# Optimization experiments

Hardware: AMD Instinct MI355X
Metric: run time of the kernel (lower is better)

Reference implementation:

```python
import jax, jax.numpy as jnp
import numpy as np

DIM = 64
N_ENTITY = 1000000
N_RELATION = 32
L = 2
B = 4096
K = 64


def setup_inputs() -> dict:
    key = jax.random.key(0)
    ks = jax.random.split(key, 24)
    s = 0.05
    d = DIM
    inp = {
        "items": jax.random.randint(ks[0], (B,), 0, N_ENTITY),
        "heads": jax.random.randint(ks[1], (L, B, K), 0, N_ENTITY),
        "relations": jax.random.randint(ks[2], (L, B, K), 0, N_RELATION),
        "tails": jax.random.randint(ks[3], (L, B, K), 0, N_ENTITY),
        # learned parameters
        "embedding": jax.random.normal(ks[4], (N_ENTITY, d), jnp.float32) * s,
        "transformer": jax.random.normal(ks[5], (N_RELATION, d), jnp.float32) * s,
        "attn_w": jax.random.normal(ks[6], (1, 3 * d), jnp.float32) * s,
        "attn_b": jax.random.normal(ks[7], (1,), jnp.float32) * s,
        "W_ih": jax.random.normal(ks[8], (d, d), jnp.float32) * s,
        "W_hh": jax.random.normal(ks[9], (d, d), jnp.float32) * s,
        "b_ih": jax.random.normal(ks[10], (d,), jnp.float32) * s,
        "b_hh": jax.random.normal(ks[11], (d,), jnp.float32) * s,
        "l1_w": jax.random.normal(ks[12], (d, 2 * d), jnp.float32) * s,
        "l1_b": jax.random.normal(ks[13], (d,), jnp.float32) * s,
        "l2_w": jax.random.normal(ks[14], (d, d), jnp.float32) * s,
        "l2_b": jax.random.normal(ks[15], (d,), jnp.float32) * s,
        "l3_w": jax.random.normal(ks[16], (d, d), jnp.float32) * s,
        "l3_b": jax.random.normal(ks[17], (d,), jnp.float32) * s,
        "lin_w": jax.random.normal(ks[18], (1, 2 * d), jnp.float32) * s,
        "lin_b": jax.random.normal(ks[19], (1,), jnp.float32) * s,
    }
    return inp


def _ncfg_forward(embedding, transformer, attn_w, attn_b, W_ih, W_hh, b_ih, b_hh,
                  l1_w, l1_b, l2_w, l2_b, l3_w, l3_b, lin_w, lin_b,
                  items, heads, relations, tails):
    o_sum = jnp.zeros((B, DIM), embedding.dtype)
    for l in range(L):
        h = embedding[heads[l]]          # [B, K, d]
        r = transformer[relations[l]]    # [B, K, d]
        tl = embedding[tails[l]]         # [B, K, d]
        hRt = jnp.concatenate([h, r, tl], axis=-1)                  # [B, K, 3d]
        pi = jax.nn.sigmoid(hRt @ attn_w.T + attn_b)                # [B, K, 1]
        pi = jax.nn.softmax(pi, axis=1)                             # softmax over neighbors
        # 2-step tanh RNN over seq (head, tail), h0 = 0
        h1 = jnp.tanh(h @ W_ih.T + b_ih + b_hh)                     # [B, K, d]
        h2 = jnp.tanh(tl @ W_ih.T + b_ih + h1 @ W_hh.T + b_hh)      # [B, K, d]
        o_sum = o_sum + (pi * h2).sum(axis=1)                       # [B, d]
    user_emb = o_sum
    item_emb = embedding[items]                                     # [B, d]
    # NCF head (dropout in eval mode = identity)
    ui = jnp.concatenate([user_emb, item_emb], axis=-1)             # [B, 2d]
    y = jax.nn.relu(ui @ l1_w.T + l1_b)
    y = jax.nn.relu(y @ l2_w.T + l2_b)
    y1 = jax.nn.sigmoid(y @ l3_w.T + l3_b)
    y2 = user_emb * item_emb
    out = jax.nn.sigmoid(jnp.concatenate([y1, y2], axis=-1) @ lin_w.T + lin_b)
    return out[:, 0]  # squeeze -> [B]


def reference(items, heads, relations, tails, embedding, transformer, attn_w, attn_b,
              W_ih, W_hh, b_ih, b_hh, l1_w, l1_b, l2_w, l2_b, l3_w, l3_b, lin_w, lin_b):
    return _ncfg_forward(embedding, transformer, attn_w, attn_b, W_ih, W_hh, b_ih, b_hh,
                         l1_w, l1_b, l2_w, l2_b, l3_w, l3_b, lin_w, lin_b,
                         items, heads, relations, tails)
```

## Files before the change

kernel.cpp:

```cpp
#include <hip/hip_runtime.h>
#include <hip/hip_bf16.h>
#include <cstdint>
#include <cstddef>

#define B_SZ 4096

typedef __attribute__((ext_vector_type(4))) float f32x4;
typedef __attribute__((ext_vector_type(8))) short sv8;
typedef __attribute__((ext_vector_type(8))) __bf16 bfv8;

__device__ __align__(16) short g_wf[2][8][64][8];
__device__ float g_bsum[64];
__device__ float g_reldot[32];

static __device__ __forceinline__ short f2bf(float x) {
  union { float f; unsigned u; } v; v.f = x;
  unsigned r = v.u + 0x7fffu + ((v.u >> 16) & 1u);
  return (short)(r >> 16);
}
static __device__ __forceinline__ short f2bfc(float x) {
  return (short)__builtin_bit_cast(unsigned short, __float2bfloat16(x));
}

static __device__ __forceinline__ f32x4 MFMA(sv8 a, sv8 b, f32x4 c) {
  return __builtin_amdgcn_mfma_f32_16x16x32_bf16(
      __builtin_bit_cast(bfv8, a), __builtin_bit_cast(bfv8, b), c, 0, 0, 0);
}

static __device__ __forceinline__ float fast_sigmoid(float x) {
  return __builtin_amdgcn_rcpf(1.f + __expf(-x));
}
static __device__ __forceinline__ float fast_tanh(float x) {
  const float e = __expf(2.f * x);
  return 1.f - 2.f * __builtin_amdgcn_rcpf(e + 1.f);
}
static __device__ __forceinline__ float dot4(f32x4 a, f32x4 b) {
  return a.x * b.x + a.y * b.y + a.z * b.z + a.w * b.w;
}
static __device__ __forceinline__ sv8 pack8(f32x4 a, f32x4 b) {
  sv8 f;
  f[0] = f2bfc(a.x); f[1] = f2bfc(a.y); f[2] = f2bfc(a.z); f[3] = f2bfc(a.w);
  f[4] = f2bfc(b.x); f[5] = f2bfc(b.y); f[6] = f2bfc(b.z); f[7] = f2bfc(b.w);
  return f;
}

__global__ __launch_bounds__(256) void ncfg_prep(
    const float* __restrict__ W_ih, const float* __restrict__ W_hh,
    const float* __restrict__ b_ih, const float* __restrict__ b_hh,
    const float* __restrict__ trf, const float* __restrict__ attn_w) {
  const int t = threadIdx.x;
  for (int q = t; q < 1024; q += 256) {
    const int m = q >> 9, f = (q >> 6) & 7, ln = q & 63;
    const int nt = f >> 1, kh = f & 1, fr = ln & 15, fg = ln >> 4;
    const float* W = m ? W_hh : W_ih;
    const float* src = W + (nt * 16 + fr) * 64 + kh * 32 + fg * 8;
    short* dst = &g_wf[m][f][ln][0];
    #pragma unroll
    for (int j = 0; j < 8; ++j) dst[j] = f2bf(src[j]);
  }
  if (t < 64) g_bsum[t] = b_ih[t] + b_hh[t];
  if (t < 32) {
    float s = 0.f;
    #pragma unroll 8
    for (int c = 0; c < 64; ++c) s += trf[t * 64 + c] * attn_w[64 + c];
    g_reldot[t] = s;
  }
}

__global__ __launch_bounds__(256, 6) void ncfg_neigh(
    const int* __restrict__ heads, const int* __restrict__ rels,
    const int* __restrict__ tails, const float* __restrict__ emb,
    const float* __restrict__ attn_w, const float* __restrict__ attn_b,
    float* __restrict__ opart) {
  const int t = threadIdx.x;
  const int lane = t & 63;
  const int w = t >> 6;
  const int fr = lane & 15;
  const int fg = lane >> 4;
  const int c0 = fg * 8;

  __shared__ __align__(16) short wlds[2][8][64][8];
  __shared__ __align__(16) float awlds[192];
  __shared__ float rlds[32];
  __shared__ __align__(16) short h1s[4][16 * 72];

  const size_t ibase = (size_t)blockIdx.x * 64;

  const int hi = heads[ibase + (w << 4) + fr];
  const int ti = tails[ibase + (w << 4) + fr];
  const int ri = rels[ibase + (w << 4) + fr];

  {
    const f32x4* s1 = (const f32x4*)&g_wf[0][0][0][0];
    f32x4* d1 = (f32x4*)&wlds[0][0][0][0];
    #pragma unroll
    for (int i = 0; i < 4; ++i) d1[t + i * 256] = s1[t + i * 256];
    if (t < 48) ((f32x4*)awlds)[t] = ((const f32x4*)attn_w)[t];
    if (t < 8) ((f32x4*)rlds)[t] = ((const f32x4*)g_reldot)[t];
  }

  float bsum[4];
  #pragma unroll
  for (int nt = 0; nt < 4; ++nt) bsum[nt] = g_bsum[nt * 16 + fr];
  const float ab0 = attn_b[0];

  const float* hr = emb + (size_t)hi * 64;
  const float* tr = emb + (size_t)ti * 64;
  const f32x4 h0 = *(const f32x4*)(hr + c0);
  const f32x4 h1 = *(const f32x4*)(hr + c0 + 4);
  const f32x4 h2 = *(const f32x4*)(hr + 32 + c0);
  const f32x4 h3 = *(const f32x4*)(hr + 32 + c0 + 4);
  const f32x4 t0 = *(const f32x4*)(tr + c0);
  const f32x4 t1 = *(const f32x4*)(tr + c0 + 4);
  const f32x4 t2 = *(const f32x4*)(tr + 32 + c0);
  const f32x4 t3 = *(const f32x4*)(tr + 32 + c0 + 4);

  __syncthreads();

  float ap = dot4(h0, *(const f32x4*)&awlds[c0]) +
             dot4(h1, *(const f32x4*)&awlds[c0 + 4]) +
             dot4(h2, *(const f32x4*)&awlds[32 + c0]) +
             dot4(h3, *(const f32x4*)&awlds[32 + c0 + 4]) +
             dot4(t0, *(const f32x4*)&awlds[128 + c0]) +
             dot4(t1, *(const f32x4*)&awlds[128 + c0 + 4]) +
             dot4(t2, *(const f32x4*)&awlds[160 + c0]) +
             dot4(t3, *(const f32x4*)&awlds[160 + c0 + 4]);
  ap += __shfl_xor(ap, 16);
  ap += __shfl_xor(ap, 32);

  const float e_own = __expf(fast_sigmoid(ap + rlds[ri] + ab0));
  float se = e_own;
  se += __shfl_xor(se, 1);
  se += __shfl_xor(se, 2);
  se += __shfl_xor(se, 4);
  se += __shfl_xor(se, 8);

  const sv8 ha0 = pack8(h0, h1), ha1 = pack8(h2, h3);
  const sv8 ta0 = pack8(t0, t1), ta1 = pack8(t2, t3);

  const f32x4 zz = {0.f, 0.f, 0.f, 0.f};

  f32x4 acc[4] = {zz, zz, zz, zz};
  #pragma unroll
  for (int nt = 0; nt < 4; ++nt)
    acc[nt] = MFMA(ha0, *(const sv8*)&wlds[0][nt * 2][lane][0], acc[nt]);
  #pragma unroll
  for (int nt = 0; nt < 4; ++nt)
    acc[nt] = MFMA(ha1, *(const sv8*)&wlds[0][nt * 2 + 1][lane][0], acc[nt]);
  #pragma unroll
  for (int nt = 0; nt < 4; ++nt)
    #pragma unroll
    for (int r = 0; r < 4; ++r)
      h1s[w][((fg << 2) + r) * 72 + nt * 16 + fr] =
          f2bfc(fast_tanh(acc[nt][r] + bsum[nt]));

  f32x4 ev;
  #pragma unroll
  for (int r = 0; r < 4; ++r) ev[r] = __shfl(e_own, (fg << 2) + r);

  f32x4 acc2[4] = {zz, zz, zz, zz};
  #pragma unroll
  for (int nt = 0; nt < 4; ++nt)
    acc2[nt] = MFMA(ta0, *(const sv8*)&wlds[0][nt * 2][lane][0], acc2[nt]);
  #pragma unroll
  for (int nt = 0; nt < 4; ++nt)
    acc2[nt] = MFMA(ta1, *(const sv8*)&wlds[0][nt * 2 + 1][lane][0], acc2[nt]);
  const sv8 a1 = *(const sv8*)&h1s[w][fr * 72 + c0];
  const sv8 a2 = *(const sv8*)&h1s[w][fr * 72 + 32 + c0];
  #pragma unroll
  for (int nt = 0; nt < 4; ++nt)
    acc2[nt] = MFMA(a1, *(const sv8*)&wlds[1][nt * 2][lane][0], acc2[nt]);
  #pragma unroll
  for (int nt = 0; nt < 4; ++nt)
    acc2[nt] = MFMA(a2, *(const sv8*)&wlds[1][nt * 2 + 1][lane][0], acc2[nt]);

  float* owp = (float*)&h1s[w][0];
  #pragma unroll
  for (int nt = 0; nt < 4; ++nt) {
    float s = ev.x * fast_tanh(acc2[nt][0] + bsum[nt]) +
              ev.y * fast_tanh(acc2[nt][1] + bsum[nt]) +
              ev.z * fast_tanh(acc2[nt][2] + bsum[nt]) +
              ev.w * fast_tanh(acc2[nt][3] + bsum[nt]);
    s += __shfl_xor(s, 16);
    s += __shfl_xor(s, 32);
    if (fg == 0) owp[nt * 16 + fr] = s;
  }
  if (lane == 0) owp[64] = se;

  __syncthreads();

  if (w == 0) {
    float o = 0.f, st = 0.f;
    #pragma unroll
    for (int q = 0; q < 4; ++q) {
      const float* p = (const float*)&h1s[q][0];
      o += p[lane];
      st += p[64];
    }
    opart[ibase + lane] = o * __builtin_amdgcn_rcpf(st);
  }
}

__global__ __launch_bounds__(256) void ncfg_head(
    const float* __restrict__ opart, const float* __restrict__ emb,
    const int* __restrict__ items, const float* __restrict__ l1_w,
    const float* __restrict__ l1_b, const float* __restrict__ l2_w,
    const float* __restrict__ l2_b, const float* __restrict__ l3_w,
    const float* __restrict__ l3_b, const float* __restrict__ lin_w,
    const float* __restrict__ lin_b, float* __restrict__ out) {
  const int wv = threadIdx.x >> 6;
  const int i = threadIdx.x & 63;
  const int b = blockIdx.x * 4 + wv;

  __shared__ float ui[4][128];
  __shared__ float yy[4][64];

  const float ue = opart[(size_t)b * 64 + i] +
                   opart[((size_t)B_SZ + b) * 64 + i];
  const float ie = emb[(size_t)items[b] * 64 + i];
  ui[wv][i] = ue;
  ui[wv][64 + i] = ie;
  __syncthreads();

  float acc = l1_b[i];
  {
    const float* wr = l1_w + i * 128;
    #pragma unroll
    for (int j = 0; j < 128; j += 4) {
      const f32x4 wvv = *(const f32x4*)(wr + j);
      const f32x4 uv = *(const f32x4*)&ui[wv][j];
      acc += wvv.x * uv.x + wvv.y * uv.y + wvv.z * uv.z + wvv.w * uv.w;
    }
  }
  float y = fmaxf(acc, 0.f);
  yy[wv][i] = y;
  __syncthreads();

  acc = l2_b[i];
  {
    const float* wr = l2_w + i * 64;
    #pragma unroll
    for (int j = 0; j < 64; j += 4) {
      const f32x4 wvv = *(const f32x4*)(wr + j);
      const f32x4 uv = *(const f32x4*)&yy[wv][j];
      acc += wvv.x * uv.x + wvv.y * uv.y + wvv.z * uv.z + wvv.w * uv.w;
    }
  }
  y = fmaxf(acc, 0.f);
  __syncthreads();
  yy[wv][i] = y;
  __syncthreads();

  acc = l3_b[i];
  {
    const float* wr = l3_w + i * 64;
    #pragma unroll
    for (int j = 0; j < 64; j += 4) {
      const f32x4 wvv = *(const f32x4*)(wr + j);
      const f32x4 uv = *(const f32x4*)&yy[wv][j];
      acc += wvv.x * uv.x + wvv.y * uv.y + wvv.z * uv.z + wvv.w * uv.w;
    }
  }
  const float y1 = fast_sigmoid(acc);
  const float y2 = ue * ie;

  float part = y1 * lin_w[i] + y2 * lin_w[64 + i];
  #pragma unroll
  for (int m = 1; m < 64; m <<= 1) part += __shfl_xor(part, m);
  if (i == 0) out[b] = fast_sigmoid(part + lin_b[0]);
}

extern "C" void kernel_launch(void* const* d_in, const int* in_sizes, int n_in,
                              void* d_out, int out_size, void* d_ws,
                              size_t ws_size, hipStream_t stream) {
  (void)in_sizes; (void)n_in; (void)out_size; (void)ws_size;
  const int* items = (const int*)d_in[0];
  const int* heads = (const int*)d_in[1];
  const int* rels = (const int*)d_in[2];
  const int* tails = (const int*)d_in[3];
  const float* emb = (const float*)d_in[4];
  const float* trf = (const float*)d_in[5];
  const float* attn_w = (const float*)d_in[6];
  const float* attn_b = (const float*)d_in[7];
  const float* W_ih = (const float*)d_in[8];
  const float* W_hh = (const float*)d_in[9];
  const float* b_ih = (const float*)d_in[10];
  const float* b_hh = (const float*)d_in[11];
  const float* l1_w = (const float*)d_in[12];
  const float* l1_b = (const float*)d_in[13];
  const float* l2_w = (const float*)d_in[14];
  const float* l2_b = (const float*)d_in[15];
  const float* l3_w = (const float*)d_in[16];
  const float* l3_b = (const float*)d_in[17];
  const float* lin_w = (const float*)d_in[18];
  const float* lin_b = (const float*)d_in[19];
  float* out = (float*)d_out;
  float* opart = (float*)d_ws;

  ncfg_prep<<<dim3(1), dim3(256), 0, stream>>>(W_ih, W_hh, b_ih, b_hh, trf,
                                               attn_w);
  ncfg_neigh<<<dim3(2 * B_SZ), dim3(256), 0, stream>>>(
      heads, rels, tails, emb, attn_w, attn_b, opart);
  ncfg_head<<<dim3(B_SZ / 4), dim3(256), 0, stream>>>(
      opart, emb, items, l1_w, l1_b, l2_w, l2_b, l3_w, l3_b, lin_w, lin_b,
      out);
}
```

Before: 84.07 us.

## Make neighbor kernel persistent per wave with software-pipelined embedding gathers

The neighbor kernel shrinks from 8192 blocks to 1024 blocks, and each wave now handles 8 chunks of 16 neighbors in a loop. The next chunk's embedding rows and indices are prefetched while the current chunk's MFMAs run, and the per-block LDS weight staging is amortised over more work. Per-chunk unnormalised weighted sums and softmax denominators go to the workspace, and the head kernel does the cross-chunk reduction and normalisation. The cost is more workspace traffic and lower occupancy (launch bounds 4), plus extra registers for the prefetched data.

```diff
diff --git a/kernel.cpp b/kernel.cpp
--- a/kernel.cpp
+++ b/kernel.cpp
@@ -67,11 +67,11 @@
   }
 }
 
-__global__ __launch_bounds__(256, 6) void ncfg_neigh(
+__global__ __launch_bounds__(256, 4) void ncfg_neigh(
     const int* __restrict__ heads, const int* __restrict__ rels,
     const int* __restrict__ tails, const float* __restrict__ emb,
     const float* __restrict__ attn_w, const float* __restrict__ attn_b,
-    float* __restrict__ opart) {
+    float* __restrict__ owp, float* __restrict__ sep) {
   const int t = threadIdx.x;
   const int lane = t & 63;
   const int w = t >> 6;
@@ -84,12 +84,6 @@
   __shared__ float rlds[32];
   __shared__ __align__(16) short h1s[4][16 * 72];
 
-  const size_t ibase = (size_t)blockIdx.x * 64;
-
-  const int hi = heads[ibase + (w << 4) + fr];
-  const int ti = tails[ibase + (w << 4) + fr];
-  const int ri = rels[ibase + (w << 4) + fr];
-
   {
     const f32x4* s1 = (const f32x4*)&g_wf[0][0][0][0];
     f32x4* d1 = (f32x4*)&wlds[0][0][0][0];
@@ -98,116 +92,139 @@
     if (t < 48) ((f32x4*)awlds)[t] = ((const f32x4*)attn_w)[t];
     if (t < 8) ((f32x4*)rlds)[t] = ((const f32x4*)g_reldot)[t];
   }
-
   float bsum[4];
   #pragma unroll
   for (int nt = 0; nt < 4; ++nt) bsum[nt] = g_bsum[nt * 16 + fr];
   const float ab0 = attn_b[0];
-
-  const float* hr = emb + (size_t)hi * 64;
-  const float* tr = emb + (size_t)ti * 64;
-  const f32x4 h0 = *(const f32x4*)(hr + c0);
-  const f32x4 h1 = *(const f32x4*)(hr + c0 + 4);
-  const f32x4 h2 = *(const f32x4*)(hr + 32 + c0);
-  const f32x4 h3 = *(const f32x4*)(hr + 32 + c0 + 4);
-  const f32x4 t0 = *(const f32x4*)(tr + c0);
-  const f32x4 t1 = *(const f32x4*)(tr + c0 + 4);
-  const f32x4 t2 = *(const f32x4*)(tr + 32 + c0);
-  const f32x4 t3 = *(const f32x4*)(tr + 32 + c0 + 4);
-
-  __syncthreads();
-
-  float ap = dot4(h0, *(const f32x4*)&awlds[c0]) +
-             dot4(h1, *(const f32x4*)&awlds[c0 + 4]) +
-             dot4(h2, *(const f32x4*)&awlds[32 + c0]) +
-             dot4(h3, *(const f32x4*)&awlds[32 + c0 + 4]) +
-             dot4(t0, *(const f32x4*)&awlds[128 + c0]) +
-             dot4(t1, *(const f32x4*)&awlds[128 + c0 + 4]) +
-             dot4(t2, *(const f32x4*)&awlds[160 + c0]) +
-             dot4(t3, *(const f32x4*)&awlds[160 + c0 + 4]);
-  ap += __shfl_xor(ap, 16);
-  ap += __shfl_xor(ap, 32);
-
-  const float e_own = __expf(fast_sigmoid(ap + rlds[ri] + ab0));
-  float se = e_own;
-  se += __shfl_xor(se, 1);
-  se += __shfl_xor(se, 2);
-  se += __shfl_xor(se, 4);
-  se += __shfl_xor(se, 8);
-
-  const sv8 ha0 = pack8(h0, h1), ha1 = pack8(h2, h3);
-  const sv8 ta0 = pack8(t0, t1), ta1 = pack8(t2, t3);
+  __syncthreads();
+
+  const int gwid = blockIdx.x * 4 + w;
+  const int cb = gwid * 8;
+
+  int hiA[2], tiA[2], riA[2];
+  hiA[0] = heads[(size_t)cb * 16 + fr];
+  tiA[0] = tails[(size_t)cb * 16 + fr];
+  riA[0] = rels[(size_t)cb * 16 + fr];
+  hiA[1] = heads[(size_t)(cb + 1) * 16 + fr];
+  tiA[1] = tails[(size_t)(cb + 1) * 16 + fr];
+  riA[1] = rels[(size_t)(cb + 1) * 16 + fr];
+
+  f32x4 gh0, gh1, gh2, gh3, gt0, gt1, gt2, gt3;
+#define LOADG(hh, tt)                                                 \
+  {                                                                   \
+    const float* hr_ = emb + (size_t)(hh)*64;                         \
+    const float* tr_ = emb + (size_t)(tt)*64;                         \
+    gh0 = *(const f32x4*)(hr_ + c0);                                  \
+    gh1 = *(const f32x4*)(hr_ + c0 + 4);                              \
+    gh2 = *(const f32x4*)(hr_ + 32 + c0);                             \
+    gh3 = *(const f32x4*)(hr_ + 32 + c0 + 4);                         \
+    gt0 = *(const f32x4*)(tr_ + c0);                                  \
+    gt1 = *(const f32x4*)(tr_ + c0 + 4);                              \
+    gt2 = *(const f32x4*)(tr_ + 32 + c0);                             \
+    gt3 = *(const f32x4*)(tr_ + 32 + c0 + 4);                         \
+  }
+
+  LOADG(hiA[0], tiA[0]);
 
   const f32x4 zz = {0.f, 0.f, 0.f, 0.f};
 
-  f32x4 acc[4] = {zz, zz, zz, zz};
-  #pragma unroll
-  for (int nt = 0; nt < 4; ++nt)
-    acc[nt] = MFMA(ha0, *(const sv8*)&wlds[0][nt * 2][lane][0], acc[nt]);
-  #pragma unroll
-  for (int nt = 0; nt < 4; ++nt)
-    acc[nt] = MFMA(ha1, *(const sv8*)&wlds[0][nt * 2 + 1][lane][0], acc[nt]);
-  #pragma unroll
-  for (int nt = 0; nt < 4; ++nt)
-    #pragma unroll
-    for (int r = 0; r < 4; ++r)
-      h1s[w][((fg << 2) + r) * 72 + nt * 16 + fr] =
-          f2bfc(fast_tanh(acc[nt][r] + bsum[nt]));
-
-  f32x4 ev;
-  #pragma unroll
-  for (int r = 0; r < 4; ++r) ev[r] = __shfl(e_own, (fg << 2) + r);
-
-  f32x4 acc2[4] = {zz, zz, zz, zz};
-  #pragma unroll
-  for (int nt = 0; nt < 4; ++nt)
-    acc2[nt] = MFMA(ta0, *(const sv8*)&wlds[0][nt * 2][lane][0], acc2[nt]);
-  #pragma unroll
-  for (int nt = 0; nt < 4; ++nt)
-    acc2[nt] = MFMA(ta1, *(const sv8*)&wlds[0][nt * 2 + 1][lane][0], acc2[nt]);
-  const sv8 a1 = *(const sv8*)&h1s[w][fr * 72 + c0];
-  const sv8 a2 = *(const sv8*)&h1s[w][fr * 72 + 32 + c0];
-  #pragma unroll
-  for (int nt = 0; nt < 4; ++nt)
-    acc2[nt] = MFMA(a1, *(const sv8*)&wlds[1][nt * 2][lane][0], acc2[nt]);
-  #pragma unroll
-  for (int nt = 0; nt < 4; ++nt)
-    acc2[nt] = MFMA(a2, *(const sv8*)&wlds[1][nt * 2 + 1][lane][0], acc2[nt]);
-
-  float* owp = (float*)&h1s[w][0];
-  #pragma unroll
-  for (int nt = 0; nt < 4; ++nt) {
-    float s = ev.x * fast_tanh(acc2[nt][0] + bsum[nt]) +
-              ev.y * fast_tanh(acc2[nt][1] + bsum[nt]) +
-              ev.z * fast_tanh(acc2[nt][2] + bsum[nt]) +
-              ev.w * fast_tanh(acc2[nt][3] + bsum[nt]);
-    s += __shfl_xor(s, 16);
-    s += __shfl_xor(s, 32);
-    if (fg == 0) owp[nt * 16 + fr] = s;
-  }
-  if (lane == 0) owp[64] = se;
-
-  __syncthreads();
-
-  if (w == 0) {
-    float o = 0.f, st = 0.f;
-    #pragma unroll
-    for (int q = 0; q < 4; ++q) {
-      const float* p = (const float*)&h1s[q][0];
-      o += p[lane];
-      st += p[64];
-    }
-    opart[ibase + lane] = o * __builtin_amdgcn_rcpf(st);
-  }
+  #pragma unroll 2
+  for (int k = 0; k < 8; ++k) {
+    const int p = k & 1;
+    const int ri_cur = riA[p];
+
+    float ap = dot4(gh0, *(const f32x4*)&awlds[c0]) +
+               dot4(gh1, *(const f32x4*)&awlds[c0 + 4]) +
+               dot4(gh2, *(const f32x4*)&awlds[32 + c0]) +
+               dot4(gh3, *(const f32x4*)&awlds[32 + c0 + 4]) +
+               dot4(gt0, *(const f32x4*)&awlds[128 + c0]) +
+               dot4(gt1, *(const f32x4*)&awlds[128 + c0 + 4]) +
+               dot4(gt2, *(const f32x4*)&awlds[160 + c0]) +
+               dot4(gt3, *(const f32x4*)&awlds[160 + c0 + 4]);
+
+    const sv8 ha0 = pack8(gh0, gh1), ha1 = pack8(gh2, gh3);
+    const sv8 ta0 = pack8(gt0, gt1), ta1 = pack8(gt2, gt3);
+
+    if (k < 7) LOADG(hiA[p ^ 1], tiA[p ^ 1]);
+    if (k < 6) {
+      hiA[p] = heads[(size_t)(cb + k + 2) * 16 + fr];
+      tiA[p] = tails[(size_t)(cb + k + 2) * 16 + fr];
+      riA[p] = rels[(size_t)(cb + k + 2) * 16 + fr];
+    }
+
+    ap += __shfl_xor(ap, 16);
+    ap += __shfl_xor(ap, 32);
+    const float e_own = __expf(fast_sigmoid(ap + rlds[ri_cur] + ab0));
+    float se = e_own;
+    se += __shfl_xor(se, 1);
+    se += __shfl_xor(se, 2);
+    se += __shfl_xor(se, 4);
+    se += __shfl_xor(se, 8);
+
+    f32x4 acc[4] = {zz, zz, zz, zz};
+    #pragma unroll
+    for (int nt = 0; nt < 4; ++nt)
+      acc[nt] = MFMA(ha0, *(const sv8*)&wlds[0][nt * 2][lane][0], acc[nt]);
+    #pragma unroll
+    for (int nt = 0; nt < 4; ++nt)
+      acc[nt] = MFMA(ha1, *(const sv8*)&wlds[0][nt * 2 + 1][lane][0], acc[nt]);
+    #pragma unroll
+    for (int nt = 0; nt < 4; ++nt)
+      #pragma unroll
+      for (int r = 0; r < 4; ++r)
+        h1s[w][((fg << 2) + r) * 72 + nt * 16 + fr] =
+            f2bfc(fast_tanh(acc[nt][r] + bsum[nt]));
+
+    f32x4 ev;
+    #pragma unroll
+    for (int r = 0; r < 4; ++r) ev[r] = __shfl(e_own, (fg << 2) + r);
+
+    f32x4 acc2[4] = {zz, zz, zz, zz};
+    #pragma unroll
+    for (int nt = 0; nt < 4; ++nt)
+      acc2[nt] = MFMA(ta0, *(const sv8*)&wlds[0][nt * 2][lane][0], acc2[nt]);
+    #pragma unroll
+    for (int nt = 0; nt < 4; ++nt)
+      acc2[nt] = MFMA(ta1, *(const sv8*)&wlds[0][nt * 2 + 1][lane][0], acc2[nt]);
+    const sv8 a1 = *(const sv8*)&h1s[w][fr * 72 + c0];
+    const sv8 a2 = *(const sv8*)&h1s[w][fr * 72 + 32 + c0];
+    #pragma unroll
+    for (int nt = 0; nt < 4; ++nt)
+      acc2[nt] = MFMA(a1, *(const sv8*)&wlds[1][nt * 2][lane][0], acc2[nt]);
+    #pragma unroll
+    for (int nt = 0; nt < 4; ++nt)
+      acc2[nt] = MFMA(a2, *(const sv8*)&wlds[1][nt * 2 + 1][lane][0], acc2[nt]);
+
+    float o4[4];
+    #pragma unroll
+    for (int nt = 0; nt < 4; ++nt) {
+      float s = ev.x * fast_tanh(acc2[nt][0] + bsum[nt]) +
+                ev.y * fast_tanh(acc2[nt][1] + bsum[nt]) +
+                ev.z * fast_tanh(acc2[nt][2] + bsum[nt]) +
+                ev.w * fast_tanh(acc2[nt][3] + bsum[nt]);
+      s += __shfl_xor(s, 16);
+      s += __shfl_xor(s, 32);
+      o4[nt] = s;
+    }
+    const float r0 = __shfl(o4[0], fr);
+    const float r1 = __shfl(o4[1], fr);
+    const float r2 = __shfl(o4[2], fr);
+    const float r3 = __shfl(o4[3], fr);
+    const float oval = (fg == 0) ? r0 : (fg == 1) ? r1 : (fg == 2) ? r2 : r3;
+    owp[(size_t)(cb + k) * 64 + lane] = oval;
+    if (lane == 0) sep[cb + k] = se;
+  }
+#undef LOADG
 }
 
 __global__ __launch_bounds__(256) void ncfg_head(
-    const float* __restrict__ opart, const float* __restrict__ emb,
-    const int* __restrict__ items, const float* __restrict__ l1_w,
-    const float* __restrict__ l1_b, const float* __restrict__ l2_w,
-    const float* __restrict__ l2_b, const float* __restrict__ l3_w,
-    const float* __restrict__ l3_b, const float* __restrict__ lin_w,
-    const float* __restrict__ lin_b, float* __restrict__ out) {
+    const float* __restrict__ owp, const float* __restrict__ sep,
+    const float* __restrict__ emb, const int* __restrict__ items,
+    const float* __restrict__ l1_w, const float* __restrict__ l1_b,
+    const float* __restrict__ l2_w, const float* __restrict__ l2_b,
+    const float* __restrict__ l3_w, const float* __restrict__ l3_b,
+    const float* __restrict__ lin_w, const float* __restrict__ lin_b,
+    float* __restrict__ out) {
   const int wv = threadIdx.x >> 6;
   const int i = threadIdx.x & 63;
   const int b = blockIdx.x * 4 + wv;
@@ -215,8 +232,16 @@
   __shared__ float ui[4][128];
   __shared__ float yy[4][64];
 
-  const float ue = opart[(size_t)b * 64 + i] +
-                   opart[((size_t)B_SZ + b) * 64 + i];
+  float u0 = 0.f, u1 = 0.f, s0 = 0.f, s1 = 0.f;
+  #pragma unroll
+  for (int s = 0; s < 4; ++s) {
+    u0 += owp[(size_t)(b * 4 + s) * 64 + i];
+    u1 += owp[(size_t)((B_SZ + b) * 4 + s) * 64 + i];
+    s0 += sep[b * 4 + s];
+    s1 += sep[(B_SZ + b) * 4 + s];
+  }
+  const float ue = u0 * __builtin_amdgcn_rcpf(s0) +
+                   u1 * __builtin_amdgcn_rcpf(s1);
   const float ie = emb[(size_t)items[b] * 64 + i];
   ui[wv][i] = ue;
   ui[wv][64 + i] = ie;
@@ -295,13 +320,14 @@
   const float* lin_w = (const float*)d_in[18];
   const float* lin_b = (const float*)d_in[19];
   float* out = (float*)d_out;
-  float* opart = (float*)d_ws;
+  float* owp = (float*)d_ws;
+  float* sep = (float*)((char*)d_ws + 8u * 1024 * 1024);
 
   ncfg_prep<<<dim3(1), dim3(256), 0, stream>>>(W_ih, W_hh, b_ih, b_hh, trf,
                                                attn_w);
-  ncfg_neigh<<<dim3(2 * B_SZ), dim3(256), 0, stream>>>(
-      heads, rels, tails, emb, attn_w, attn_b, opart);
+  ncfg_neigh<<<dim3(1024), dim3(256), 0, stream>>>(
+      heads, rels, tails, emb, attn_w, attn_b, owp, sep);
   ncfg_head<<<dim3(B_SZ / 4), dim3(256), 0, stream>>>(
-      opart, emb, items, l1_w, l1_b, l2_w, l2_b, l3_w, l3_b, lin_w, lin_b,
+      owp, sep, emb, items, l1_w, l1_b, l2_w, l2_b, l3_w, l3_b, lin_w, lin_b,
       out);
 }
```

After: 222.6 us. +164.8%, slower.
